# Optimization experiments

Measured on AMD Instinct MI355X. Metric: run time of the kernel, lower is better.

The kernel has to match this reference:

```python
import jax, jax.numpy as jnp
import numpy as np

B, C, L = 1024, 256, 16   # nodes, channels (num_features), num_ell (dim of 0e+1o+2e+3o)
E = 10                    # num_elements
K3, K2, K1 = 23, 4, 1     # U-matrix path counts for correlation orders 3,2,1


def setup_inputs() -> dict:
    key = jax.random.key(0)
    ks = jax.random.split(key, 8)
    return {
        "x": jax.random.normal(ks[0], (B, C, L), jnp.float32),
        "y": jax.random.normal(ks[1], (B, E), jnp.float32),
        # U buffers (generalized Clebsch-Gordan, here random stand-ins of the right shapes)
        "U3": jax.random.normal(ks[2], (L, L, L, K3), jnp.float32),
        "U2": jax.random.normal(ks[3], (L, L, K2), jnp.float32),
        "U1": jax.random.normal(ks[4], (L, K1), jnp.float32),
        # per-element weights, scaled by 1/num_params as in the module
        "W3": jax.random.normal(ks[5], (E, K3, C), jnp.float32) / K3,
        "W2": jax.random.normal(ks[6], (E, K2, C), jnp.float32) / K2,
        "W1": jax.random.normal(ks[7], (E, K1, C), jnp.float32) / K1,
    }


def reference(x, y, U3, U2, U1, W3, W2, W1):
    # symmetric_cp, irrep_out lmax=0 (scalar output), correlation=3.
    # Main (nu=3): out[b,c,w,v] = sum_{i,k,e} U3[w,v,i,k] W3[e,k,c] x[b,c,i] y[b,e]
    # Efficient order: element-select weights, outer-product over (i,k), then one GEMM with U3.
    w3 = jnp.einsum('ekc,be->bkc', W3, y)              # [B,K3,C]
    q = jnp.einsum('bkc,bci->bcik', w3, x)             # [B,C,L,K3]
    out = jnp.einsum('wvik,bcik->bcwv', U3, q)         # [B,C,L,L]
    # nu=2: weighting then feature contraction
    w2 = jnp.einsum('ekc,be->bkc', W2, y)              # [B,K2,C]
    c2 = jnp.einsum('wvk,bkc->bcwv', U2, w2) + out     # [B,C,L,L]
    out = jnp.einsum('bcwi,bci->bcw', c2, x)           # [B,C,L]
    # nu=1
    w1 = jnp.einsum('ekc,be->bkc', W1, y)              # [B,K1,C]
    c1 = jnp.einsum('wk,bkc->bcw', U1, w1) + out       # [B,C,L]
    out = jnp.einsum('bci,bci->bc', c1, x)             # [B,C]
    return out.reshape(out.shape[0], -1)
```

## Files before the change

kernel.cpp:

```cpp
#include <hip/hip_runtime.h>


#define B_   1024
#define C_   256
#define L_   16
#define E_   10
#define K3_  23
#define K2_  4

#define NM3  816
#define NM2  136
#define MTOT 992
#define NCH2 61
#define STSTR 68

using f32x4   = __attribute__((ext_vector_type(4))) float;
using f32x16  = __attribute__((ext_vector_type(16))) float;
using short8v = __attribute__((ext_vector_type(8))) short;

__device__ __host__ __forceinline__ constexpr int tri_(int n) { return n * (n + 1) / 2; }
__device__ __host__ __forceinline__ constexpr int tet_(int n) { return n * (n + 1) * (n + 2) / 6; }

struct MTab { unsigned char a[MTOT], b[MTOT], c[MTOT]; };
constexpr MTab mkMT() {
  MTab t = {};
  int m = 0;
  for (int a = 0; a < 16; a++)
    for (int b = a; b < 16; b++)
      for (int c = b; c < 16; c++) { t.a[m] = a; t.b[m] = b; t.c[m] = c; ++m; }
  for (int a = 0; a < 16; a++)
    for (int b = a; b < 16; b++) { t.a[m] = a; t.b[m] = b; t.c[m] = 16; ++m; }
  for (int a = 0; a < 16; a++) { t.a[m] = a; t.b[m] = 16; t.c[m] = 16; ++m; }
  while (m < MTOT) { t.a[m] = 17; t.b[m] = 17; t.c[m] = 17; ++m; }
  return t;
}
constexpr MTab MT = mkMT();

__global__ void prep_kernel(const float* __restrict__ U3, const float* __restrict__ U2,
                            const float* __restrict__ U1, unsigned short* __restrict__ wsFrag) {
  __shared__ float sRow[16][36];
  const int ch = blockIdx.x;
  const int tid = threadIdx.x;
  if (tid < 16) {
    const int m = ch * 16 + tid;
    for (int i = 0; i < 36; i++) sRow[tid][i] = 0.f;
    if (m < NM3) {
      int ia = 0;
      while (tet_(16) - tet_(16 - (ia + 1)) <= m) ia++;
      int rem = m - (tet_(16) - tet_(16 - ia));
      int ib = ia;
      while (tri_(16 - ia) - tri_(16 - (ib + 1)) <= rem) ib++;
      int ic = ib + (rem - (tri_(16 - ia) - tri_(16 - ib)));
      int pw[6] = {ia, ia, ib, ib, ic, ic};
      int pv[6] = {ib, ic, ia, ic, ia, ib};
      int pi[6] = {ic, ib, ic, ia, ib, ia};
      bool use[6];
      for (int p = 0; p < 6; p++) {
        bool dup = false;
        for (int q = 0; q < p; q++)
          dup = dup || (pw[p] == pw[q] && pv[p] == pv[q] && pi[p] == pi[q]);
        use[p] = !dup;
      }
      for (int k = 0; k < K3_; k++) {
        float s = 0.f;
        for (int p = 0; p < 6; p++)
          if (use[p]) s += U3[((pw[p] * L_ + pv[p]) * L_ + pi[p]) * K3_ + k];
        sRow[tid][k] = s;
      }
    } else if (m < NM3 + NM2) {
      const int pidx = m - NM3;
      int ia = 0;
      while (136 - tri_(16 - (ia + 1)) <= pidx) ia++;
      int ib = ia + (pidx - (136 - tri_(16 - ia)));
      for (int k2 = 0; k2 < K2_; k2++) {
        float s = U2[(ia * L_ + ib) * K2_ + k2];
        if (ia != ib) s += U2[(ib * L_ + ia) * K2_ + k2];
        sRow[tid][23 + k2] = s;
      }
    } else if (m < NM3 + NM2 + L_) {
      sRow[tid][27] = U1[m - NM3 - NM2];
    }
  }
  __syncthreads();
  {
    const int lane = tid & 63, part = tid >> 6;
    unsigned short v16[8];
    for (int j = 0; j < 8; j++) {
      float v = sRow[(lane >> 5) * 8 + j][lane & 31];
      unsigned vb = __float_as_uint(v);
      unsigned short h = (unsigned short)(vb >> 16);
      if (part == 0) {
        v16[j] = h;
      } else {
        float lres = v - __uint_as_float(((unsigned)h) << 16);
        v16[j] = (unsigned short)(__float_as_uint(lres) >> 16);
      }
    }
    unsigned* dst = (unsigned*)(wsFrag + ((size_t)(ch * 2 + part) * 64 + lane) * 8);
    for (int p = 0; p < 4; p++)
      dst[p] = (unsigned)v16[2 * p] | ((unsigned)v16[2 * p + 1] << 16);
  }
}

__device__ __forceinline__ void lane32_swap(unsigned& a, unsigned& b) {
#if defined(__has_builtin) && __has_builtin(__builtin_amdgcn_permlane32_swap)
  auto r = __builtin_amdgcn_permlane32_swap((int)a, (int)b, false, false);
  a = (unsigned)r[0];
  b = (unsigned)r[1];
#else
  asm volatile("v_permlane32_swap_b32 %0, %1" : "+v"(a), "+v"(b));
#endif
}

template <int CH>
__device__ __forceinline__ void chunk_body(
    const float (&XX)[18], const float4* __restrict__ Bg, int lane,
    float4& nbH0, float4& nbL0, float4& nbH1, float4& nbL1,
    f32x16& acc0, f32x16& acc1) {
  unsigned pk0[4], pk1[4];
  #pragma unroll
  for (int i = 0; i < 4; ++i) {
    {
      const int m0 = CH * 16 + 2 * i;
      float p0 = XX[MT.a[m0]] * XX[MT.b[m0]] * XX[MT.c[m0]];
      float p1 = XX[MT.a[m0 + 1]] * XX[MT.b[m0 + 1]] * XX[MT.c[m0 + 1]];
      asm("v_cvt_pk_bf16_f32 %0, %1, %2" : "=v"(pk0[i]) : "v"(p0), "v"(p1));
    }
    {
      const int m0 = CH * 16 + 8 + 2 * i;
      float p0 = XX[MT.a[m0]] * XX[MT.b[m0]] * XX[MT.c[m0]];
      float p1 = XX[MT.a[m0 + 1]] * XX[MT.b[m0 + 1]] * XX[MT.c[m0 + 1]];
      asm("v_cvt_pk_bf16_f32 %0, %1, %2" : "=v"(pk1[i]) : "v"(p0), "v"(p1));
    }
    lane32_swap(pk0[i], pk1[i]);
  }

  float4 bh, bl;
  if constexpr ((CH & 1) == 0) { bh = nbH0; bl = nbL0; } else { bh = nbH1; bl = nbL1; }
  if constexpr (CH + 2 < NCH2) {
    if constexpr ((CH & 1) == 0) {
      nbH0 = Bg[(CH + 2) * 128 + lane];
      nbL0 = Bg[(CH + 2) * 128 + 64 + lane];
    } else {
      nbH1 = Bg[(CH + 2) * 128 + lane];
      nbL1 = Bg[(CH + 2) * 128 + 64 + lane];
    }
  }
  short8v A0, A1, BH, BL;
  __builtin_memcpy(&A0, pk0, 16);
  __builtin_memcpy(&A1, pk1, 16);
  __builtin_memcpy(&BH, &bh, 16);
  __builtin_memcpy(&BL, &bl, 16);

  acc0 = __builtin_amdgcn_mfma_f32_32x32x16_bf16(A0, BH, acc0, 0, 0, 0);
  acc1 = __builtin_amdgcn_mfma_f32_32x32x16_bf16(A1, BH, acc1, 0, 0, 0);
  acc0 = __builtin_amdgcn_mfma_f32_32x32x16_bf16(A0, BL, acc0, 0, 0, 0);
  acc1 = __builtin_amdgcn_mfma_f32_32x32x16_bf16(A1, BL, acc1, 0, 0, 0);
}

template <int CH>
struct Loop {
  static __device__ __forceinline__ void run(
      const float (&XX)[18], const float4* __restrict__ Bg, int lane,
      float4& nbH0, float4& nbL0, float4& nbH1, float4& nbL1,
      f32x16& acc0, f32x16& acc1) {
    chunk_body<CH>(XX, Bg, lane, nbH0, nbL0, nbH1, nbL1, acc0, acc1);
    Loop<CH + 1>::run(XX, Bg, lane, nbH0, nbL0, nbH1, nbL1, acc0, acc1);
  }
};
template <>
struct Loop<NCH2> {
  static __device__ __forceinline__ void run(
      const float (&)[18], const float4* __restrict__, int,
      float4&, float4&, float4&, float4&, f32x16&, f32x16&) {}
};

__global__ __launch_bounds__(64, 2) void symcon_kernel(
    const float* __restrict__ x,
    const float* __restrict__ y,
    const float* __restrict__ W3,
    const float* __restrict__ W2,
    const float* __restrict__ W1,
    const unsigned short* __restrict__ wsFrag,
    float* __restrict__ out)
{
  __shared__ __attribute__((aligned(16))) float sT[28 * STSTR];

  const int lane = threadIdx.x;
  const int bb = blockIdx.x;
  const int b = bb >> 2;
  const int c = (bb & 3) * 64 + lane;

  float XX[18];
  {
    const float4* xg = (const float4*)(x + ((size_t)b * C_ + c) * L_);
    #pragma unroll
    for (int i = 0; i < 4; i++) {
      float4 v = xg[i];
      XX[i * 4 + 0] = v.x; XX[i * 4 + 1] = v.y;
      XX[i * 4 + 2] = v.z; XX[i * 4 + 3] = v.w;
    }
    XX[16] = 1.f; XX[17] = 0.f;
  }

  const float4* Bg = (const float4*)wsFrag;
  float4 nbH0 = Bg[lane],        nbL0 = Bg[64 + lane];
  float4 nbH1 = Bg[128 + lane],  nbL1 = Bg[192 + lane];
  f32x16 acc0 = (f32x16)0.f, acc1 = (f32x16)0.f;

  Loop<0>::run(XX, Bg, lane, nbH0, nbL0, nbH1, nbL1, acc0, acc1);

  const int kcol = lane & 31, hi = lane >> 5;
  if (kcol < 28) {
    #pragma unroll
    for (int q = 0; q < 4; ++q) {
      f32x4 v0, v1;
      #pragma unroll
      for (int i2 = 0; i2 < 4; ++i2) {
        v0[i2] = acc0[4 * q + i2];
        v1[i2] = acc1[4 * q + i2];
      }
      *(f32x4*)&sT[kcol * STSTR +      8 * q + 4 * hi] = v0;
      *(f32x4*)&sT[kcol * STSTR + 32 + 8 * q + 4 * hi] = v1;
    }
  }
  float t[28];
  #pragma unroll
  for (int k = 0; k < 28; ++k) t[k] = sT[k * STSTR + lane];

  float yreg[E_];
  #pragma unroll
  for (int e = 0; e < E_; e++) yreg[e] = y[b * E_ + e];

  float result = 0.f;
  #pragma unroll
  for (int k = 0; k < K3_; k++) {
    const float* w3p = &W3[k * C_ + c];
    float w3k = 0.f;
    #pragma unroll
    for (int e = 0; e < E_; e++) w3k += w3p[e * K3_ * C_] * yreg[e];
    result += t[k] * w3k;
  }
  #pragma unroll
  for (int k2 = 0; k2 < K2_; k2++) {
    const float* w2p = &W2[k2 * C_ + c];
    float w2k = 0.f;
    #pragma unroll
    for (int e = 0; e < E_; e++) w2k += w2p[e * K2_ * C_] * yreg[e];
    result += t[23 + k2] * w2k;
  }
  {
    float w1v = 0.f;
    #pragma unroll
    for (int e = 0; e < E_; e++) w1v += W1[e * C_ + c] * yreg[e];
    result += t[27] * w1v;
  }

  out[(size_t)b * C_ + c] = result;
}

extern "C" void kernel_launch(void* const* d_in, const int* in_sizes, int n_in,
                              void* d_out, int out_size, void* d_ws, size_t ws_size,
                              hipStream_t stream) {
  const float* x  = (const float*)d_in[0];
  const float* y  = (const float*)d_in[1];
  const float* U3 = (const float*)d_in[2];
  const float* U2 = (const float*)d_in[3];
  const float* U1 = (const float*)d_in[4];
  const float* W3 = (const float*)d_in[5];
  const float* W2 = (const float*)d_in[6];
  const float* W1 = (const float*)d_in[7];
  float* out = (float*)d_out;

  unsigned short* wsFrag = (unsigned short*)d_ws;

  prep_kernel<<<dim3(NCH2), dim3(128), 0, stream>>>(U3, U2, U1, wsFrag);
  symcon_kernel<<<dim3(B_ * 4), dim3(64), 0, stream>>>(
      x, y, W3, W2, W1, wsFrag, out);
}
```

Before: 129.7 us.

## Drop bf16 hi/lo split of U fragments and specialize monomial products at compile time

The U-matrix B operand was split into high and low bf16 parts, which took two MFMAs per A tile to reach near-fp32 precision. It is now a single round-to-nearest bf16 value, so MFMA count and B-fragment loads per chunk are halved. Monomial products are also specialized at compile time, so padding entries and lower-order terms skip the multiplies by the constants 1 and 0. The cost is lower accuracy, since the U coefficients now carry only bf16 precision, which could push the result outside tolerance.

```diff
diff --git a/kernel.cpp b/kernel.cpp
--- a/kernel.cpp
+++ b/kernel.cpp
@@ -83,20 +83,14 @@
   }
   __syncthreads();
   {
-    const int lane = tid & 63, part = tid >> 6;
+    const int lane = tid;
     unsigned short v16[8];
     for (int j = 0; j < 8; j++) {
       float v = sRow[(lane >> 5) * 8 + j][lane & 31];
-      unsigned vb = __float_as_uint(v);
-      unsigned short h = (unsigned short)(vb >> 16);
-      if (part == 0) {
-        v16[j] = h;
-      } else {
-        float lres = v - __uint_as_float(((unsigned)h) << 16);
-        v16[j] = (unsigned short)(__float_as_uint(lres) >> 16);
-      }
-    }
-    unsigned* dst = (unsigned*)(wsFrag + ((size_t)(ch * 2 + part) * 64 + lane) * 8);
+      unsigned vb = __float_as_uint(v) + 0x8000u;
+      v16[j] = (unsigned short)(vb >> 16);
+    }
+    unsigned* dst = (unsigned*)(wsFrag + ((size_t)ch * 64 + lane) * 8);
     for (int p = 0; p < 4; p++)
       dst[p] = (unsigned)v16[2 * p] | ((unsigned)v16[2 * p + 1] << 16);
   }
@@ -112,67 +106,69 @@
 #endif
 }
 
+template <int M>
+__device__ __forceinline__ float pval(const float (&XX)[16]) {
+  if constexpr (MT.a[M] == 17) return 0.f;
+  else if constexpr (MT.b[M] == 16) return XX[MT.a[M]];
+  else if constexpr (MT.c[M] == 16) return XX[MT.a[M]] * XX[MT.b[M]];
+  else return XX[MT.a[M]] * XX[MT.b[M]] * XX[MT.c[M]];
+}
+
+template <int CH, int I>
+__device__ __forceinline__ void pk_pair(const float (&XX)[16],
+                                        unsigned& o0, unsigned& o1) {
+  {
+    float p0 = pval<CH * 16 + 2 * I>(XX);
+    float p1 = pval<CH * 16 + 2 * I + 1>(XX);
+    asm("v_cvt_pk_bf16_f32 %0, %1, %2" : "=v"(o0) : "v"(p0), "v"(p1));
+  }
+  {
+    float p0 = pval<CH * 16 + 8 + 2 * I>(XX);
+    float p1 = pval<CH * 16 + 8 + 2 * I + 1>(XX);
+    asm("v_cvt_pk_bf16_f32 %0, %1, %2" : "=v"(o1) : "v"(p0), "v"(p1));
+  }
+  lane32_swap(o0, o1);
+}
+
 template <int CH>
 __device__ __forceinline__ void chunk_body(
-    const float (&XX)[18], const float4* __restrict__ Bg, int lane,
-    float4& nbH0, float4& nbL0, float4& nbH1, float4& nbL1,
-    f32x16& acc0, f32x16& acc1) {
+    const float (&XX)[16], const float4* __restrict__ Bg, int lane,
+    float4& nb0, float4& nb1, f32x16& acc0, f32x16& acc1) {
   unsigned pk0[4], pk1[4];
-  #pragma unroll
-  for (int i = 0; i < 4; ++i) {
-    {
-      const int m0 = CH * 16 + 2 * i;
-      float p0 = XX[MT.a[m0]] * XX[MT.b[m0]] * XX[MT.c[m0]];
-      float p1 = XX[MT.a[m0 + 1]] * XX[MT.b[m0 + 1]] * XX[MT.c[m0 + 1]];
-      asm("v_cvt_pk_bf16_f32 %0, %1, %2" : "=v"(pk0[i]) : "v"(p0), "v"(p1));
-    }
-    {
-      const int m0 = CH * 16 + 8 + 2 * i;
-      float p0 = XX[MT.a[m0]] * XX[MT.b[m0]] * XX[MT.c[m0]];
-      float p1 = XX[MT.a[m0 + 1]] * XX[MT.b[m0 + 1]] * XX[MT.c[m0 + 1]];
-      asm("v_cvt_pk_bf16_f32 %0, %1, %2" : "=v"(pk1[i]) : "v"(p0), "v"(p1));
-    }
-    lane32_swap(pk0[i], pk1[i]);
-  }
-
-  float4 bh, bl;
-  if constexpr ((CH & 1) == 0) { bh = nbH0; bl = nbL0; } else { bh = nbH1; bl = nbL1; }
+  pk_pair<CH, 0>(XX, pk0[0], pk1[0]);
+  pk_pair<CH, 1>(XX, pk0[1], pk1[1]);
+  pk_pair<CH, 2>(XX, pk0[2], pk1[2]);
+  pk_pair<CH, 3>(XX, pk0[3], pk1[3]);
+
+  float4 bh;
+  if constexpr ((CH & 1) == 0) bh = nb0; else bh = nb1;
   if constexpr (CH + 2 < NCH2) {
-    if constexpr ((CH & 1) == 0) {
-      nbH0 = Bg[(CH + 2) * 128 + lane];
-      nbL0 = Bg[(CH + 2) * 128 + 64 + lane];
-    } else {
-      nbH1 = Bg[(CH + 2) * 128 + lane];
-      nbL1 = Bg[(CH + 2) * 128 + 64 + lane];
-    }
-  }
-  short8v A0, A1, BH, BL;
+    if constexpr ((CH & 1) == 0) nb0 = Bg[(CH + 2) * 64 + lane];
+    else                         nb1 = Bg[(CH + 2) * 64 + lane];
+  }
+  short8v A0, A1, BH;
   __builtin_memcpy(&A0, pk0, 16);
   __builtin_memcpy(&A1, pk1, 16);
   __builtin_memcpy(&BH, &bh, 16);
-  __builtin_memcpy(&BL, &bl, 16);
 
   acc0 = __builtin_amdgcn_mfma_f32_32x32x16_bf16(A0, BH, acc0, 0, 0, 0);
   acc1 = __builtin_amdgcn_mfma_f32_32x32x16_bf16(A1, BH, acc1, 0, 0, 0);
-  acc0 = __builtin_amdgcn_mfma_f32_32x32x16_bf16(A0, BL, acc0, 0, 0, 0);
-  acc1 = __builtin_amdgcn_mfma_f32_32x32x16_bf16(A1, BL, acc1, 0, 0, 0);
 }
 
 template <int CH>
 struct Loop {
   static __device__ __forceinline__ void run(
-      const float (&XX)[18], const float4* __restrict__ Bg, int lane,
-      float4& nbH0, float4& nbL0, float4& nbH1, float4& nbL1,
-      f32x16& acc0, f32x16& acc1) {
-    chunk_body<CH>(XX, Bg, lane, nbH0, nbL0, nbH1, nbL1, acc0, acc1);
-    Loop<CH + 1>::run(XX, Bg, lane, nbH0, nbL0, nbH1, nbL1, acc0, acc1);
+      const float (&XX)[16], const float4* __restrict__ Bg, int lane,
+      float4& nb0, float4& nb1, f32x16& acc0, f32x16& acc1) {
+    chunk_body<CH>(XX, Bg, lane, nb0, nb1, acc0, acc1);
+    Loop<CH + 1>::run(XX, Bg, lane, nb0, nb1, acc0, acc1);
   }
 };
 template <>
 struct Loop<NCH2> {
   static __device__ __forceinline__ void run(
-      const float (&)[18], const float4* __restrict__, int,
-      float4&, float4&, float4&, float4&, f32x16&, f32x16&) {}
+      const float (&)[16], const float4* __restrict__, int,
+      float4&, float4&, f32x16&, f32x16&) {}
 };
 
 __global__ __launch_bounds__(64, 2) void symcon_kernel(
@@ -191,7 +187,7 @@
   const int b = bb >> 2;
   const int c = (bb & 3) * 64 + lane;
 
-  float XX[18];
+  float XX[16];
   {
     const float4* xg = (const float4*)(x + ((size_t)b * C_ + c) * L_);
     #pragma unroll
@@ -200,15 +196,13 @@
       XX[i * 4 + 0] = v.x; XX[i * 4 + 1] = v.y;
       XX[i * 4 + 2] = v.z; XX[i * 4 + 3] = v.w;
     }
-    XX[16] = 1.f; XX[17] = 0.f;
   }
 
   const float4* Bg = (const float4*)wsFrag;
-  float4 nbH0 = Bg[lane],        nbL0 = Bg[64 + lane];
-  float4 nbH1 = Bg[128 + lane],  nbL1 = Bg[192 + lane];
+  float4 nb0 = Bg[lane], nb1 = Bg[64 + lane];
   f32x16 acc0 = (f32x16)0.f, acc1 = (f32x16)0.f;
 
-  Loop<0>::run(XX, Bg, lane, nbH0, nbL0, nbH1, nbL1, acc0, acc1);
+  Loop<0>::run(XX, Bg, lane, nb0, nb1, acc0, acc1);
 
   const int kcol = lane & 31, hi = lane >> 5;
   if (kcol < 28) {
@@ -274,7 +268,7 @@
 
   unsigned short* wsFrag = (unsigned short*)d_ws;
 
-  prep_kernel<<<dim3(NCH2), dim3(128), 0, stream>>>(U3, U2, U1, wsFrag);
+  prep_kernel<<<dim3(NCH2), dim3(64), 0, stream>>>(U3, U2, U1, wsFrag);
   symcon_kernel<<<dim3(B_ * 4), dim3(64), 0, stream>>>(
       x, y, W3, W2, W1, wsFrag, out);
 }
```

After: 119.2 us. 1.09x faster.
